# Kernel tuning notes

Hardware: AMD Instinct MI355X
Metric: run time of the kernel (lower is better)

The kernel has to match this reference:

```python
import jax, jax.numpy as jnp
import numpy as np

N = 50000
E = 800000
D_IN = 256
D_OUT = 256
EPS = 1.0 + 1e-06


def setup_inputs() -> dict:
    key = jax.random.key(0)
    ks = jax.random.split(key, 10)
    x = jax.random.normal(ks[0], (N, D_IN), dtype=jnp.float32)
    lower_indices = jax.random.randint(ks[1], (2, E), 0, N, dtype=jnp.int64)
    lower_values = jax.random.uniform(ks[2], (E,), dtype=jnp.float32)
    upper_indices = jax.random.randint(ks[3], (2, E), 0, N, dtype=jnp.int64)
    upper_values = jax.random.uniform(ks[4], (E,), dtype=jnp.float32)
    s = 1.0 / np.sqrt(D_IN)
    W_lower = jax.random.uniform(ks[5], (D_IN, D_OUT), jnp.float32, -s, s)
    att_lower = jax.random.uniform(ks[6], (2 * D_OUT,), jnp.float32, -s, s)
    W_upper = jax.random.uniform(ks[7], (D_IN, D_OUT), jnp.float32, -s, s)
    att_upper = jax.random.uniform(ks[8], (2 * D_OUT,), jnp.float32, -s, s)
    W_lin = jax.random.uniform(ks[9], (D_IN, D_OUT), jnp.float32, -s, s)
    return {"x": x, "lower_indices": lower_indices, "lower_values": lower_values,
            "upper_indices": upper_indices, "upper_values": upper_values,
            "W_lower": W_lower, "att_lower": att_lower,
            "W_upper": W_upper, "att_upper": att_upper, "W_lin": W_lin}


def can_conv(x, indices, values, W, att_weight):
    # x: [N, d_in]; indices: [2, E] (row=target i, col=source j); values: [E]
    n = x.shape[0]
    xm = x @ W                                    # [N, d_out]
    tgt, src = indices[0], indices[1]
    d = xm.shape[1]
    # attention: elu( [x_i ; x_j] . att_weight ) computed without concat
    score = jax.nn.elu(xm @ att_weight[:d])[tgt] + jax.nn.elu(0.0) * 0.0  # placeholder
    score = jax.nn.elu((xm @ att_weight[:d])[tgt] + (xm @ att_weight[d:])[src])  # [E]
    v = score * values                            # attention * neighborhood values
    # sparse row-wise softmax (per target index)
    m = jax.ops.segment_max(v, tgt, num_segments=n)
    e = jnp.exp(v - m[tgt])
    s = jax.ops.segment_sum(e, tgt, num_segments=n)
    a = e / s[tgt]                                # [E]
    # spmm: out[i] = sum_j a_ij * xm[j]
    return jax.ops.segment_sum(a[:, None] * xm[src], tgt, num_segments=n)


def reference(x, lower_indices, lower_values, upper_indices, upper_values,
              W_lower, att_lower, W_upper, att_upper, W_lin):
    lower_x = can_conv(x, lower_indices, lower_values, W_lower, att_lower)
    upper_x = can_conv(x, upper_indices, upper_values, W_upper, att_upper)
    w_x = (x @ W_lin) * EPS
    return jax.nn.relu(lower_x + upper_x + w_x)
```

## Files before the change

kernel.cpp:

```cpp
#include <hip/hip_runtime.h>
#include <hip/hip_bf16.h>


constexpr int N_NODES = 50000;
constexpr int N_EDGES = 800000;
constexpr int D = 256;
constexpr float EPSV = 1.0f + 1e-06f;

typedef __attribute__((ext_vector_type(8))) short short8;
typedef __attribute__((ext_vector_type(4))) float f32x4;

__device__ __forceinline__ unsigned short f2bf(float f) {
    unsigned int b = __float_as_uint(f);
    unsigned int r = (b + 0x7FFFu + ((b >> 16) & 1u)) >> 16;
    return (unsigned short)r;
}
__device__ __forceinline__ float bf2f(unsigned short u) {
    return __uint_as_float(((unsigned int)u) << 16);
}

__global__ __launch_bounds__(256) void prep_kernel(
    const float4* __restrict__ x, ushort4* __restrict__ xb, int n4,
    const float* __restrict__ W0, const float* __restrict__ W1,
    const float* __restrict__ W2, unsigned short* __restrict__ wbT,
    const int* __restrict__ il, const int* __restrict__ iu,
    int* __restrict__ cl, int* __restrict__ cu,
    int* __restrict__ rkl, int* __restrict__ rku)
{
    int gid = blockIdx.x * 256 + threadIdx.x;
    int gsz = gridDim.x * 256;
    for (int i = gid; i < n4; i += gsz) {
        float4 v = x[i];
        ushort4 o;
        o.x = f2bf(v.x); o.y = f2bf(v.y); o.z = f2bf(v.z); o.w = f2bf(v.w);
        xb[i] = o;
    }
    for (int i = gid; i < 3 * 65536; i += gsz) {
        int z = i >> 16, rem = i & 65535;
        int k = rem >> 8, n = rem & 255;
        const float* W = (z == 0) ? W0 : (z == 1) ? W1 : W2;
        wbT[(size_t)z * 65536 + (size_t)n * 256 + k] = f2bf(W[(size_t)k * 256 + n]);
    }
    for (int e = gid; e < N_EDGES; e += gsz) {
        rkl[e] = atomicAdd(&cl[il[e]], 1);
        rku[e] = atomicAdd(&cu[iu[e]], 1);
    }
}

__global__ __launch_bounds__(256) void gemm_lds_kernel(
    const unsigned short* __restrict__ xb, const unsigned short* __restrict__ wbT,
    unsigned short* __restrict__ xml, unsigned short* __restrict__ xmu,
    float* __restrict__ out, int M)
{
    const int wz = blockIdx.z;
    const int tid = threadIdx.x;
    const int w = tid >> 6, lane = tid & 63;
    const int r16 = lane & 15, g = lane >> 4;
    const int m0 = blockIdx.x * 128 + w * 32;
    const int n0 = blockIdx.y * 64;

    __shared__ short8 bs[8][4][64];
    {
        const unsigned short* wb = wbT + (size_t)wz * 65536;
        #pragma unroll
        for (int c = tid; c < 2048; c += 256) {
            int kt = c >> 8, nf = (c >> 6) & 3, l = c & 63;
            bs[kt][nf][l] = *reinterpret_cast<const short8*>(
                wb + (size_t)(n0 + nf * 16 + (l & 15)) * 256 + kt * 32 + 8 * (l >> 4));
        }
    }
    __syncthreads();

    const int ar0 = min(m0 + r16, M - 1);
    const int ar1 = min(m0 + 16 + r16, M - 1);
    const unsigned short* pa0 = xb + (size_t)ar0 * 256 + 8 * g;
    const unsigned short* pa1 = xb + (size_t)ar1 * 256 + 8 * g;

    f32x4 acc[2][4];
    #pragma unroll
    for (int mf = 0; mf < 2; ++mf)
        #pragma unroll
        for (int nf = 0; nf < 4; ++nf)
            acc[mf][nf] = (f32x4){0.f, 0.f, 0.f, 0.f};

    #pragma unroll
    for (int kt = 0; kt < 8; ++kt) {
        short8 a0 = *reinterpret_cast<const short8*>(pa0 + kt * 32);
        short8 a1 = *reinterpret_cast<const short8*>(pa1 + kt * 32);
        #pragma unroll
        for (int nf = 0; nf < 4; ++nf) {
            short8 bf = bs[kt][nf][lane];
            acc[0][nf] = __builtin_amdgcn_mfma_f32_16x16x32_bf16(a0, bf, acc[0][nf], 0, 0, 0);
            acc[1][nf] = __builtin_amdgcn_mfma_f32_16x16x32_bf16(a1, bf, acc[1][nf], 0, 0, 0);
        }
    }

    if (wz < 2) {
        unsigned short* dst = wz ? xmu : xml;
        #pragma unroll
        for (int mf = 0; mf < 2; ++mf)
            #pragma unroll
            for (int r = 0; r < 4; ++r) {
                int row = m0 + mf * 16 + g * 4 + r;
                if (row < M) {
                    #pragma unroll
                    for (int nf = 0; nf < 4; ++nf)
                        dst[(size_t)row * 256 + n0 + nf * 16 + r16] = f2bf(acc[mf][nf][r]);
                }
            }
    } else {
        #pragma unroll
        for (int mf = 0; mf < 2; ++mf)
            #pragma unroll
            for (int r = 0; r < 4; ++r) {
                int row = m0 + mf * 16 + g * 4 + r;
                if (row < M) {
                    #pragma unroll
                    for (int nf = 0; nf < 4; ++nf)
                        out[(size_t)row * 256 + n0 + nf * 16 + r16] = acc[mf][nf][r] * EPSV;
                }
            }
    }
}

__global__ __launch_bounds__(256) void att_both_kernel(
    const unsigned short* __restrict__ xml, const unsigned short* __restrict__ xmu,
    const float* __restrict__ att_l, const float* __restrict__ att_u,
    float* __restrict__ al, float* __restrict__ bl,
    float* __restrict__ au, float* __restrict__ bu, int n)
{
    int node = (int)((blockIdx.x * 256 + threadIdx.x) >> 6);
    int lane = threadIdx.x & 63;
    if (node >= n) return;
    int o = lane * 4;
    ushort4 ul = *reinterpret_cast<const ushort4*>(xml + (size_t)node * 256 + o);
    ushort4 uu = *reinterpret_cast<const ushort4*>(xmu + (size_t)node * 256 + o);
    float l0 = bf2f(ul.x), l1 = bf2f(ul.y), l2 = bf2f(ul.z), l3 = bf2f(ul.w);
    float u0 = bf2f(uu.x), u1 = bf2f(uu.y), u2 = bf2f(uu.z), u3 = bf2f(uu.w);
    float p[4];
    p[0] = l0 * att_l[o] + l1 * att_l[o + 1] + l2 * att_l[o + 2] + l3 * att_l[o + 3];
    p[1] = l0 * att_l[D + o] + l1 * att_l[D + o + 1] + l2 * att_l[D + o + 2] + l3 * att_l[D + o + 3];
    p[2] = u0 * att_u[o] + u1 * att_u[o + 1] + u2 * att_u[o + 2] + u3 * att_u[o + 3];
    p[3] = u0 * att_u[D + o] + u1 * att_u[D + o + 1] + u2 * att_u[D + o + 2] + u3 * att_u[D + o + 3];
    #pragma unroll
    for (int off = 32; off; off >>= 1)
        #pragma unroll
        for (int c = 0; c < 4; ++c)
            p[c] += __shfl_down(p[c], off);
    if (lane == 0) { al[node] = p[0]; bl[node] = p[1]; au[node] = p[2]; bu[node] = p[3]; }
}

__global__ __launch_bounds__(1024) void scan_local_kernel(
    const int* __restrict__ cnt0, int* __restrict__ ro0,
    const int* __restrict__ cnt1, int* __restrict__ ro1,
    int* __restrict__ bsum, int n)
{
    int c = blockIdx.y;
    const int* cnt = c ? cnt1 : cnt0;
    int* ro = c ? ro1 : ro0;
    __shared__ int sm[1024];
    int tid = threadIdx.x;
    int i = blockIdx.x * 1024 + tid;
    int v = (i < n) ? cnt[i] : 0;
    sm[tid] = v;
    __syncthreads();
    #pragma unroll
    for (int off = 1; off < 1024; off <<= 1) {
        int t = (tid >= off) ? sm[tid - off] : 0;
        __syncthreads();
        sm[tid] += t;
        __syncthreads();
    }
    if (i < n) ro[i] = sm[tid] - v;
    if (tid == 1023) bsum[c * 64 + blockIdx.x] = sm[1023];
}

__global__ __launch_bounds__(128) void scan_bsum_kernel(int* __restrict__ bsum, int nb)
{
    int c = threadIdx.x >> 6, lane = threadIdx.x & 63;
    int v = (lane < nb) ? bsum[c * 64 + lane] : 0;
    int orig = v;
    #pragma unroll
    for (int off = 1; off < 64; off <<= 1) {
        int t = __shfl_up(v, off);
        if (lane >= off) v += t;
    }
    if (lane < nb) bsum[c * 64 + lane] = v - orig;
}

__global__ __launch_bounds__(256) void scan_apply_kernel(
    int* __restrict__ ro0, int* __restrict__ ro1,
    const int* __restrict__ bsum, int n)
{
    int c = blockIdx.y;
    int* ro = c ? ro1 : ro0;
    int i = blockIdx.x * 256 + threadIdx.x;
    if (i < n) ro[i] += bsum[c * 64 + (i >> 10)];
    if (i == 0) ro[n] = N_EDGES;
}

__global__ __launch_bounds__(256) void scatter_kernel(
    const int* __restrict__ il, const float* __restrict__ vl,
    const int* __restrict__ rol, const int* __restrict__ rkl, int2* __restrict__ egl,
    const int* __restrict__ iu, const float* __restrict__ vu,
    const int* __restrict__ rou, const int* __restrict__ rku, int2* __restrict__ egu)
{
    int e = blockIdx.x * 256 + threadIdx.x;
    if (e >= N_EDGES) return;
    int2 p; p.x = il[N_EDGES + e]; p.y = __float_as_int(vl[e]);
    egl[rol[il[e]] + rkl[e]] = p;
    int2 q; q.x = iu[N_EDGES + e]; q.y = __float_as_int(vu[e]);
    egu[rou[iu[e]] + rku[e]] = q;
}

__device__ __forceinline__ float wave_sum(float v) {
    #pragma unroll
    for (int off = 32; off; off >>= 1) v += __shfl_xor(v, off);
    return v;
}

__device__ __forceinline__ void pv_accum(
    int lane, float invs, float evl, int srcl, int m,
    const unsigned short* __restrict__ xm, float4& acc)
{
    int t = 0;
    for (; t + 2 <= m; t += 2) {
        float w0 = __shfl(evl, t) * invs;
        int   s0 = __shfl(srcl, t);
        float w1 = __shfl(evl, t + 1) * invs;
        int   s1 = __shfl(srcl, t + 1);
        ushort4 u0 = *reinterpret_cast<const ushort4*>(xm + (size_t)s0 * 256 + lane * 4);
        ushort4 u1 = *reinterpret_cast<const ushort4*>(xm + (size_t)s1 * 256 + lane * 4);
        acc.x += w0 * bf2f(u0.x) + w1 * bf2f(u1.x);
        acc.y += w0 * bf2f(u0.y) + w1 * bf2f(u1.y);
        acc.z += w0 * bf2f(u0.z) + w1 * bf2f(u1.z);
        acc.w += w0 * bf2f(u0.w) + w1 * bf2f(u1.w);
    }
    if (t < m) {
        float w0 = __shfl(evl, t) * invs;
        int   s0 = __shfl(srcl, t);
        ushort4 u0 = *reinterpret_cast<const ushort4*>(xm + (size_t)s0 * 256 + lane * 4);
        acc.x += w0 * bf2f(u0.x);
        acc.y += w0 * bf2f(u0.y);
        acc.z += w0 * bf2f(u0.z);
        acc.w += w0 * bf2f(u0.w);
    }
}

__device__ __forceinline__ void conv_accum(
    int node, int lane,
    const int* __restrict__ ro, const int2* __restrict__ eg,
    const float* __restrict__ a, const float* __restrict__ b,
    const unsigned short* __restrict__ xm, float4& acc)
{
    int rs = ro[node], re = ro[node + 1];
    int deg = re - rs;
    if (deg <= 0) return;
    float ai = a[node];
    if (deg <= 64) {
        float evl = 0.f; int srcl = 0;
        if (lane < deg) {
            int2 p = eg[rs + lane];
            srcl = p.x;
            float xv = ai + b[srcl];
            float sc = (xv > 0.f) ? xv : (expf(xv) - 1.f);
            evl = expf(sc * __int_as_float(p.y));
        }
        float invs = 1.f / wave_sum(evl);
        pv_accum(lane, invs, evl, srcl, deg, xm, acc);
    } else {
        float s = 0.f;
        for (int c = rs; c < re; c += 64) {
            int m = min(64, re - c);
            float evl = 0.f;
            if (lane < m) {
                int2 p = eg[c + lane];
                float xv = ai + b[p.x];
                float sc = (xv > 0.f) ? xv : (expf(xv) - 1.f);
                evl = expf(sc * __int_as_float(p.y));
            }
            s += wave_sum(evl);
        }
        float invs = 1.f / s;
        for (int c = rs; c < re; c += 64) {
            int m = min(64, re - c);
            float evl = 0.f; int srcl = 0;
            if (lane < m) {
                int2 p = eg[c + lane];
                srcl = p.x;
                float xv = ai + b[srcl];
                float sc = (xv > 0.f) ? xv : (expf(xv) - 1.f);
                evl = expf(sc * __int_as_float(p.y));
            }
            pv_accum(lane, invs, evl, srcl, m, xm, acc);
        }
    }
}

__global__ __launch_bounds__(256) void gather_kernel(
    const int* __restrict__ rol, const int2* __restrict__ egl,
    const float* __restrict__ al, const float* __restrict__ bl,
    const unsigned short* __restrict__ xml,
    const int* __restrict__ rou, const int2* __restrict__ egu,
    const float* __restrict__ au, const float* __restrict__ bu,
    const unsigned short* __restrict__ xmu,
    float4* __restrict__ out)
{
    int node = (int)((blockIdx.x * 256 + threadIdx.x) >> 6);
    int lane = threadIdx.x & 63;
    if (node >= N_NODES) return;
    float4 acc = make_float4(0.f, 0.f, 0.f, 0.f);
    conv_accum(node, lane, rol, egl, al, bl, xml, acc);
    conv_accum(node, lane, rou, egu, au, bu, xmu, acc);
    float4 xw = out[(size_t)node * 64 + lane];
    acc.x = fmaxf(acc.x + xw.x, 0.f);
    acc.y = fmaxf(acc.y + xw.y, 0.f);
    acc.z = fmaxf(acc.z + xw.z, 0.f);
    acc.w = fmaxf(acc.w + xw.w, 0.f);
    out[(size_t)node * 64 + lane] = acc;
}

extern "C" void kernel_launch(void* const* d_in, const int* in_sizes, int n_in,
                              void* d_out, int out_size, void* d_ws, size_t ws_size,
                              hipStream_t stream)
{
    (void)in_sizes; (void)n_in; (void)out_size; (void)ws_size;
    const float* x        = (const float*)d_in[0];
    const int*   low_idx  = (const int*)  d_in[1];
    const float* low_vals = (const float*)d_in[2];
    const int*   up_idx   = (const int*)  d_in[3];
    const float* up_vals  = (const float*)d_in[4];
    const float* W_lower  = (const float*)d_in[5];
    const float* att_low  = (const float*)d_in[6];
    const float* W_upper  = (const float*)d_in[7];
    const float* att_up   = (const float*)d_in[8];
    const float* W_lin    = (const float*)d_in[9];
    float* out = (float*)d_out;

    char* ws = (char*)d_ws;
    size_t off = 0;
    auto alloc = [&](size_t bytes) {
        void* p = ws + off;
        off += (bytes + 255) & ~(size_t)255;
        return p;
    };
    unsigned short* xb     = (unsigned short*)alloc((size_t)N_NODES * D * 2);
    unsigned short* wbT    = (unsigned short*)alloc((size_t)3 * 256 * 256 * 2);
    unsigned short* xm_low = (unsigned short*)alloc((size_t)N_NODES * D * 2);
    unsigned short* xm_up  = (unsigned short*)alloc((size_t)N_NODES * D * 2);
    float* a_low  = (float*)alloc(N_NODES * 4);
    float* b_low  = (float*)alloc(N_NODES * 4);
    float* a_up   = (float*)alloc(N_NODES * 4);
    float* b_up   = (float*)alloc(N_NODES * 4);
    int* zero_blk = (int*)alloc(2 * N_NODES * 4);
    int* cnt_low = zero_blk;
    int* cnt_up  = zero_blk + N_NODES;
    int* rk_low  = (int*)alloc((size_t)N_EDGES * 4);
    int* rk_up   = (int*)alloc((size_t)N_EDGES * 4);
    int* ro_low  = (int*)alloc((N_NODES + 1) * 4);
    int* ro_up   = (int*)alloc((N_NODES + 1) * 4);
    int* bsum    = (int*)alloc(2 * 64 * 4);
    int2* eg_low = (int2*)alloc((size_t)N_EDGES * 8);
    int2* eg_up  = (int2*)alloc((size_t)N_EDGES * 8);

    hipMemsetAsync(zero_blk, 0, 2 * N_NODES * 4, stream);

    int n4 = N_NODES * D / 4;
    prep_kernel<<<2048, 256, 0, stream>>>(
        (const float4*)x, (ushort4*)xb, n4,
        W_lower, W_upper, W_lin, wbT,
        low_idx, up_idx, cnt_low, cnt_up, rk_low, rk_up);

    dim3 ggrid((N_NODES + 127) / 128, 4, 3);
    gemm_lds_kernel<<<ggrid, 256, 0, stream>>>(xb, wbT, xm_low, xm_up, out, N_NODES);

    int ablocks = (N_NODES + 3) / 4;
    att_both_kernel<<<ablocks, 256, 0, stream>>>(
        xm_low, xm_up, att_low, att_up, a_low, b_low, a_up, b_up, N_NODES);

    dim3 sgrid((N_NODES + 1023) / 1024, 2);
    scan_local_kernel<<<sgrid, 1024, 0, stream>>>(cnt_low, ro_low, cnt_up, ro_up,
                                                  bsum, N_NODES);
    scan_bsum_kernel<<<1, 128, 0, stream>>>(bsum, (N_NODES + 1023) / 1024);
    dim3 agrid((N_NODES + 255) / 256, 2);
    scan_apply_kernel<<<agrid, 256, 0, stream>>>(ro_low, ro_up, bsum, N_NODES);
    int eblocks = (N_EDGES + 255) / 256;
    scatter_kernel<<<eblocks, 256, 0, stream>>>(
        low_idx, low_vals, ro_low, rk_low, eg_low,
        up_idx,  up_vals,  ro_up,  rk_up,  eg_up);

    int gblocks = (N_NODES + 3) / 4;
    gather_kernel<<<gblocks, 256, 0, stream>>>(
        ro_low, eg_low, a_low, b_low, xm_low,
        ro_up,  eg_up,  a_up,  b_up,  xm_up,
        (float4*)out);
}
```

Before: 439.4 us.

## Fuse scan passes, merge attention with scatter, bf16 skip path, split gather waves

The three-kernel scan is replaced by a single decoupled-lookback scan that spins on per-block flags. The attention-score kernel and the edge scatter kernel are merged into one launch. The skip GEMM now writes a bf16 buffer instead of fp32 into the output, which cuts write and read traffic. The gather kernel gives the lower and upper convolutions separate waves and reduces them through LDS, and the gather inner loop is unrolled to four edges. The trade-offs are a spin-wait that assumes all scan blocks are co-resident, and bf16 rounding on the skip term.

```diff
diff --git a/kernel.cpp b/kernel.cpp
--- a/kernel.cpp
+++ b/kernel.cpp
@@ -50,7 +50,7 @@
 __global__ __launch_bounds__(256) void gemm_lds_kernel(
     const unsigned short* __restrict__ xb, const unsigned short* __restrict__ wbT,
     unsigned short* __restrict__ xml, unsigned short* __restrict__ xmu,
-    float* __restrict__ out, int M)
+    unsigned short* __restrict__ skipb, int M)
 {
     const int wz = blockIdx.z;
     const int tid = threadIdx.x;
@@ -95,72 +95,34 @@
         }
     }
 
-    if (wz < 2) {
-        unsigned short* dst = wz ? xmu : xml;
-        #pragma unroll
-        for (int mf = 0; mf < 2; ++mf)
-            #pragma unroll
-            for (int r = 0; r < 4; ++r) {
-                int row = m0 + mf * 16 + g * 4 + r;
-                if (row < M) {
-                    #pragma unroll
-                    for (int nf = 0; nf < 4; ++nf)
-                        dst[(size_t)row * 256 + n0 + nf * 16 + r16] = f2bf(acc[mf][nf][r]);
-                }
+    unsigned short* dst = (wz == 0) ? xml : (wz == 1) ? xmu : skipb;
+    const float scale = (wz == 2) ? EPSV : 1.0f;
+    #pragma unroll
+    for (int mf = 0; mf < 2; ++mf)
+        #pragma unroll
+        for (int r = 0; r < 4; ++r) {
+            int row = m0 + mf * 16 + g * 4 + r;
+            if (row < M) {
+                #pragma unroll
+                for (int nf = 0; nf < 4; ++nf)
+                    dst[(size_t)row * 256 + n0 + nf * 16 + r16] = f2bf(acc[mf][nf][r] * scale);
             }
-    } else {
-        #pragma unroll
-        for (int mf = 0; mf < 2; ++mf)
-            #pragma unroll
-            for (int r = 0; r < 4; ++r) {
-                int row = m0 + mf * 16 + g * 4 + r;
-                if (row < M) {
-                    #pragma unroll
-                    for (int nf = 0; nf < 4; ++nf)
-                        out[(size_t)row * 256 + n0 + nf * 16 + r16] = acc[mf][nf][r] * EPSV;
-                }
-            }
-    }
-}
-
-__global__ __launch_bounds__(256) void att_both_kernel(
-    const unsigned short* __restrict__ xml, const unsigned short* __restrict__ xmu,
-    const float* __restrict__ att_l, const float* __restrict__ att_u,
-    float* __restrict__ al, float* __restrict__ bl,
-    float* __restrict__ au, float* __restrict__ bu, int n)
-{
-    int node = (int)((blockIdx.x * 256 + threadIdx.x) >> 6);
-    int lane = threadIdx.x & 63;
-    if (node >= n) return;
-    int o = lane * 4;
-    ushort4 ul = *reinterpret_cast<const ushort4*>(xml + (size_t)node * 256 + o);
-    ushort4 uu = *reinterpret_cast<const ushort4*>(xmu + (size_t)node * 256 + o);
-    float l0 = bf2f(ul.x), l1 = bf2f(ul.y), l2 = bf2f(ul.z), l3 = bf2f(ul.w);
-    float u0 = bf2f(uu.x), u1 = bf2f(uu.y), u2 = bf2f(uu.z), u3 = bf2f(uu.w);
-    float p[4];
-    p[0] = l0 * att_l[o] + l1 * att_l[o + 1] + l2 * att_l[o + 2] + l3 * att_l[o + 3];
-    p[1] = l0 * att_l[D + o] + l1 * att_l[D + o + 1] + l2 * att_l[D + o + 2] + l3 * att_l[D + o + 3];
-    p[2] = u0 * att_u[o] + u1 * att_u[o + 1] + u2 * att_u[o + 2] + u3 * att_u[o + 3];
-    p[3] = u0 * att_u[D + o] + u1 * att_u[D + o + 1] + u2 * att_u[D + o + 2] + u3 * att_u[D + o + 3];
-    #pragma unroll
-    for (int off = 32; off; off >>= 1)
-        #pragma unroll
-        for (int c = 0; c < 4; ++c)
-            p[c] += __shfl_down(p[c], off);
-    if (lane == 0) { al[node] = p[0]; bl[node] = p[1]; au[node] = p[2]; bu[node] = p[3]; }
-}
-
-__global__ __launch_bounds__(1024) void scan_local_kernel(
+        }
+}
+
+__global__ __launch_bounds__(1024) void scan_kernel(
     const int* __restrict__ cnt0, int* __restrict__ ro0,
     const int* __restrict__ cnt1, int* __restrict__ ro1,
-    int* __restrict__ bsum, int n)
+    int* __restrict__ fv, int n)
 {
     int c = blockIdx.y;
     const int* cnt = c ? cnt1 : cnt0;
     int* ro = c ? ro1 : ro0;
+    int b = blockIdx.x;
     __shared__ int sm[1024];
+    __shared__ int s_prefix;
     int tid = threadIdx.x;
-    int i = blockIdx.x * 1024 + tid;
+    int i = b * 1024 + tid;
     int v = (i < n) ? cnt[i] : 0;
     sm[tid] = v;
     __syncthreads();
@@ -171,46 +133,64 @@
         sm[tid] += t;
         __syncthreads();
     }
-    if (i < n) ro[i] = sm[tid] - v;
-    if (tid == 1023) bsum[c * 64 + blockIdx.x] = sm[1023];
-}
-
-__global__ __launch_bounds__(128) void scan_bsum_kernel(int* __restrict__ bsum, int nb)
-{
-    int c = threadIdx.x >> 6, lane = threadIdx.x & 63;
-    int v = (lane < nb) ? bsum[c * 64 + lane] : 0;
-    int orig = v;
-    #pragma unroll
-    for (int off = 1; off < 64; off <<= 1) {
-        int t = __shfl_up(v, off);
-        if (lane >= off) v += t;
-    }
-    if (lane < nb) bsum[c * 64 + lane] = v - orig;
-}
-
-__global__ __launch_bounds__(256) void scan_apply_kernel(
-    int* __restrict__ ro0, int* __restrict__ ro1,
-    const int* __restrict__ bsum, int n)
-{
-    int c = blockIdx.y;
-    int* ro = c ? ro1 : ro0;
-    int i = blockIdx.x * 256 + threadIdx.x;
-    if (i < n) ro[i] += bsum[c * 64 + (i >> 10)];
-    if (i == 0) ro[n] = N_EDGES;
-}
-
-__global__ __launch_bounds__(256) void scatter_kernel(
+    int total = sm[1023];
+    if (tid == 0) atomicExch(&fv[c * 64 + b], total + 1);
+    if (tid < 64) {
+        int p = 0;
+        if (tid < b) {
+            int f;
+            while ((f = atomicAdd(&fv[c * 64 + tid], 0)) == 0) {}
+            p = f - 1;
+        }
+        #pragma unroll
+        for (int off = 32; off; off >>= 1) p += __shfl_xor(p, off);
+        if (tid == 0) s_prefix = p;
+    }
+    __syncthreads();
+    int prefix = s_prefix;
+    if (i < n) ro[i] = prefix + sm[tid] - v;
+    if (tid == 0 && b == (int)gridDim.x - 1) ro[n] = prefix + total;
+}
+
+__global__ __launch_bounds__(256) void att_scatter_kernel(
+    const unsigned short* __restrict__ xml, const unsigned short* __restrict__ xmu,
+    const float* __restrict__ att_l, const float* __restrict__ att_u,
+    float* __restrict__ al, float* __restrict__ bl,
+    float* __restrict__ au, float* __restrict__ bu, int n_ab,
     const int* __restrict__ il, const float* __restrict__ vl,
     const int* __restrict__ rol, const int* __restrict__ rkl, int2* __restrict__ egl,
     const int* __restrict__ iu, const float* __restrict__ vu,
     const int* __restrict__ rou, const int* __restrict__ rku, int2* __restrict__ egu)
 {
-    int e = blockIdx.x * 256 + threadIdx.x;
-    if (e >= N_EDGES) return;
-    int2 p; p.x = il[N_EDGES + e]; p.y = __float_as_int(vl[e]);
-    egl[rol[il[e]] + rkl[e]] = p;
-    int2 q; q.x = iu[N_EDGES + e]; q.y = __float_as_int(vu[e]);
-    egu[rou[iu[e]] + rku[e]] = q;
+    int bx = (int)blockIdx.x;
+    if (bx < n_ab) {
+        int node = (int)((bx * 256 + threadIdx.x) >> 6);
+        int lane = threadIdx.x & 63;
+        if (node >= N_NODES) return;
+        int o = lane * 4;
+        ushort4 ul = *reinterpret_cast<const ushort4*>(xml + (size_t)node * 256 + o);
+        ushort4 uu = *reinterpret_cast<const ushort4*>(xmu + (size_t)node * 256 + o);
+        float l0 = bf2f(ul.x), l1 = bf2f(ul.y), l2 = bf2f(ul.z), l3 = bf2f(ul.w);
+        float u0 = bf2f(uu.x), u1 = bf2f(uu.y), u2 = bf2f(uu.z), u3 = bf2f(uu.w);
+        float p[4];
+        p[0] = l0 * att_l[o] + l1 * att_l[o + 1] + l2 * att_l[o + 2] + l3 * att_l[o + 3];
+        p[1] = l0 * att_l[D + o] + l1 * att_l[D + o + 1] + l2 * att_l[D + o + 2] + l3 * att_l[D + o + 3];
+        p[2] = u0 * att_u[o] + u1 * att_u[o + 1] + u2 * att_u[o + 2] + u3 * att_u[o + 3];
+        p[3] = u0 * att_u[D + o] + u1 * att_u[D + o + 1] + u2 * att_u[D + o + 2] + u3 * att_u[D + o + 3];
+        #pragma unroll
+        for (int off = 32; off; off >>= 1)
+            #pragma unroll
+            for (int c = 0; c < 4; ++c)
+                p[c] += __shfl_down(p[c], off);
+        if (lane == 0) { al[node] = p[0]; bl[node] = p[1]; au[node] = p[2]; bu[node] = p[3]; }
+    } else {
+        int e = (bx - n_ab) * 256 + threadIdx.x;
+        if (e >= N_EDGES) return;
+        int2 p; p.x = il[N_EDGES + e]; p.y = __float_as_int(vl[e]);
+        egl[rol[il[e]] + rkl[e]] = p;
+        int2 q; q.x = iu[N_EDGES + e]; q.y = __float_as_int(vu[e]);
+        egu[rou[iu[e]] + rku[e]] = q;
+    }
 }
 
 __device__ __forceinline__ float wave_sum(float v) {
@@ -224,19 +204,25 @@
     const unsigned short* __restrict__ xm, float4& acc)
 {
     int t = 0;
-    for (; t + 2 <= m; t += 2) {
-        float w0 = __shfl(evl, t) * invs;
-        int   s0 = __shfl(srcl, t);
+    for (; t + 4 <= m; t += 4) {
+        float w0 = __shfl(evl, t)     * invs;
         float w1 = __shfl(evl, t + 1) * invs;
-        int   s1 = __shfl(srcl, t + 1);
+        float w2 = __shfl(evl, t + 2) * invs;
+        float w3 = __shfl(evl, t + 3) * invs;
+        int s0 = __shfl(srcl, t);
+        int s1 = __shfl(srcl, t + 1);
+        int s2 = __shfl(srcl, t + 2);
+        int s3 = __shfl(srcl, t + 3);
         ushort4 u0 = *reinterpret_cast<const ushort4*>(xm + (size_t)s0 * 256 + lane * 4);
         ushort4 u1 = *reinterpret_cast<const ushort4*>(xm + (size_t)s1 * 256 + lane * 4);
-        acc.x += w0 * bf2f(u0.x) + w1 * bf2f(u1.x);
-        acc.y += w0 * bf2f(u0.y) + w1 * bf2f(u1.y);
-        acc.z += w0 * bf2f(u0.z) + w1 * bf2f(u1.z);
-        acc.w += w0 * bf2f(u0.w) + w1 * bf2f(u1.w);
-    }
-    if (t < m) {
+        ushort4 u2 = *reinterpret_cast<const ushort4*>(xm + (size_t)s2 * 256 + lane * 4);
+        ushort4 u3 = *reinterpret_cast<const ushort4*>(xm + (size_t)s3 * 256 + lane * 4);
+        acc.x += w0 * bf2f(u0.x) + w1 * bf2f(u1.x) + w2 * bf2f(u2.x) + w3 * bf2f(u3.x);
+        acc.y += w0 * bf2f(u0.y) + w1 * bf2f(u1.y) + w2 * bf2f(u2.y) + w3 * bf2f(u3.y);
+        acc.z += w0 * bf2f(u0.z) + w1 * bf2f(u1.z) + w2 * bf2f(u2.z) + w3 * bf2f(u3.z);
+        acc.w += w0 * bf2f(u0.w) + w1 * bf2f(u1.w) + w2 * bf2f(u2.w) + w3 * bf2f(u3.w);
+    }
+    for (; t < m; ++t) {
         float w0 = __shfl(evl, t) * invs;
         int   s0 = __shfl(srcl, t);
         ushort4 u0 = *reinterpret_cast<const ushort4*>(xm + (size_t)s0 * 256 + lane * 4);
@@ -304,20 +290,30 @@
     const int* __restrict__ rou, const int2* __restrict__ egu,
     const float* __restrict__ au, const float* __restrict__ bu,
     const unsigned short* __restrict__ xmu,
-    float4* __restrict__ out)
-{
-    int node = (int)((blockIdx.x * 256 + threadIdx.x) >> 6);
-    int lane = threadIdx.x & 63;
-    if (node >= N_NODES) return;
+    const unsigned short* __restrict__ skipb, float4* __restrict__ out)
+{
+    int tid = threadIdx.x;
+    int slot = tid >> 7;
+    int conv = (tid >> 6) & 1;
+    int lane = tid & 63;
+    int node = blockIdx.x * 2 + slot;
+    __shared__ float4 red[2][64];
     float4 acc = make_float4(0.f, 0.f, 0.f, 0.f);
-    conv_accum(node, lane, rol, egl, al, bl, xml, acc);
-    conv_accum(node, lane, rou, egu, au, bu, xmu, acc);
-    float4 xw = out[(size_t)node * 64 + lane];
-    acc.x = fmaxf(acc.x + xw.x, 0.f);
-    acc.y = fmaxf(acc.y + xw.y, 0.f);
-    acc.z = fmaxf(acc.z + xw.z, 0.f);
-    acc.w = fmaxf(acc.w + xw.w, 0.f);
-    out[(size_t)node * 64 + lane] = acc;
+    if (node < N_NODES) {
+        if (conv == 0) conv_accum(node, lane, rol, egl, al, bl, xml, acc);
+        else           conv_accum(node, lane, rou, egu, au, bu, xmu, acc);
+    }
+    if (conv == 1) red[slot][lane] = acc;
+    __syncthreads();
+    if (conv == 0 && node < N_NODES) {
+        float4 o = red[slot][lane];
+        ushort4 sk = *reinterpret_cast<const ushort4*>(skipb + (size_t)node * 256 + lane * 4);
+        acc.x = fmaxf(acc.x + o.x + bf2f(sk.x), 0.f);
+        acc.y = fmaxf(acc.y + o.y + bf2f(sk.y), 0.f);
+        acc.z = fmaxf(acc.z + o.z + bf2f(sk.z), 0.f);
+        acc.w = fmaxf(acc.w + o.w + bf2f(sk.w), 0.f);
+        out[(size_t)node * 64 + lane] = acc;
+    }
 }
 
 extern "C" void kernel_launch(void* const* d_in, const int* in_sizes, int n_in,
@@ -348,22 +344,23 @@
     unsigned short* wbT    = (unsigned short*)alloc((size_t)3 * 256 * 256 * 2);
     unsigned short* xm_low = (unsigned short*)alloc((size_t)N_NODES * D * 2);
     unsigned short* xm_up  = (unsigned short*)alloc((size_t)N_NODES * D * 2);
+    unsigned short* skipb  = (unsigned short*)alloc((size_t)N_NODES * D * 2);
     float* a_low  = (float*)alloc(N_NODES * 4);
     float* b_low  = (float*)alloc(N_NODES * 4);
     float* a_up   = (float*)alloc(N_NODES * 4);
     float* b_up   = (float*)alloc(N_NODES * 4);
-    int* zero_blk = (int*)alloc(2 * N_NODES * 4);
+    int* zero_blk = (int*)alloc((2 * N_NODES + 128) * 4);
     int* cnt_low = zero_blk;
     int* cnt_up  = zero_blk + N_NODES;
+    int* fv      = zero_blk + 2 * N_NODES;
     int* rk_low  = (int*)alloc((size_t)N_EDGES * 4);
     int* rk_up   = (int*)alloc((size_t)N_EDGES * 4);
     int* ro_low  = (int*)alloc((N_NODES + 1) * 4);
     int* ro_up   = (int*)alloc((N_NODES + 1) * 4);
-    int* bsum    = (int*)alloc(2 * 64 * 4);
     int2* eg_low = (int2*)alloc((size_t)N_EDGES * 8);
     int2* eg_up  = (int2*)alloc((size_t)N_EDGES * 8);
 
-    hipMemsetAsync(zero_blk, 0, 2 * N_NODES * 4, stream);
+    hipMemsetAsync(zero_blk, 0, (2 * N_NODES + 128) * 4, stream);
 
     int n4 = N_NODES * D / 4;
     prep_kernel<<<2048, 256, 0, stream>>>(
@@ -372,26 +369,21 @@
         low_idx, up_idx, cnt_low, cnt_up, rk_low, rk_up);
 
     dim3 ggrid((N_NODES + 127) / 128, 4, 3);
-    gemm_lds_kernel<<<ggrid, 256, 0, stream>>>(xb, wbT, xm_low, xm_up, out, N_NODES);
+    gemm_lds_kernel<<<ggrid, 256, 0, stream>>>(xb, wbT, xm_low, xm_up, skipb, N_NODES);
+
+    dim3 sgrid((N_NODES + 1023) / 1024, 2);
+    scan_kernel<<<sgrid, 1024, 0, stream>>>(cnt_low, ro_low, cnt_up, ro_up, fv, N_NODES);
 
     int ablocks = (N_NODES + 3) / 4;
-    att_both_kernel<<<ablocks, 256, 0, stream>>>(
-        xm_low, xm_up, att_low, att_up, a_low, b_low, a_up, b_up, N_NODES);
-
-    dim3 sgrid((N_NODES + 1023) / 1024, 2);
-    scan_local_kernel<<<sgrid, 1024, 0, stream>>>(cnt_low, ro_low, cnt_up, ro_up,
-                                                  bsum, N_NODES);
-    scan_bsum_kernel<<<1, 128, 0, stream>>>(bsum, (N_NODES + 1023) / 1024);
-    dim3 agrid((N_NODES + 255) / 256, 2);
-    scan_apply_kernel<<<agrid, 256, 0, stream>>>(ro_low, ro_up, bsum, N_NODES);
     int eblocks = (N_EDGES + 255) / 256;
-    scatter_kernel<<<eblocks, 256, 0, stream>>>(
+    att_scatter_kernel<<<ablocks + eblocks, 256, 0, stream>>>(
+        xm_low, xm_up, att_low, att_up, a_low, b_low, a_up, b_up, ablocks,
         low_idx, low_vals, ro_low, rk_low, eg_low,
         up_idx,  up_vals,  ro_up,  rk_up,  eg_up);
 
-    int gblocks = (N_NODES + 3) / 4;
+    int gblocks = (N_NODES + 1) / 2;
     gather_kernel<<<gblocks, 256, 0, stream>>>(
         ro_low, eg_low, a_low, b_low, xm_low,
         ro_up,  eg_up,  a_up,  b_up,  xm_up,
-        (float4*)out);
-}
+        skipb, (float4*)out);
+}
```

After: 454.7 us. 3.5% more time.

## Fuse three GEMMs per block, precompute edge exps in scatter, split gather per conv

Applied to the files above, without the earlier changes.

The GEMM now loads each A tile into registers once and loops over the three weight matrices, so the x tile is not re-read per matrix. The skip projection is written as bf16 to a scratch buffer instead of fp32 into the output. The scatter kernel computes the ELU/exp edge weights up front, so the gather no longer does per-edge attention math and random reads of b. The gather assigns one wave per conv per node, sums the two results through LDS, and unrolls the SpMM by four. Storing the skip term in bf16 adds rounding error and removes one fp32 read-modify-write of the output. The exp is taken without subtracting the segment max, which could overflow for large scores.

```diff
diff --git a/kernel.cpp b/kernel.cpp
--- a/kernel.cpp
+++ b/kernel.cpp
@@ -47,12 +47,11 @@
     }
 }
 
-__global__ __launch_bounds__(256) void gemm_lds_kernel(
+__global__ __launch_bounds__(256) void gemm_zreg_kernel(
     const unsigned short* __restrict__ xb, const unsigned short* __restrict__ wbT,
     unsigned short* __restrict__ xml, unsigned short* __restrict__ xmu,
-    float* __restrict__ out, int M)
-{
-    const int wz = blockIdx.z;
+    unsigned short* __restrict__ skipb, int M)
+{
     const int tid = threadIdx.x;
     const int w = tid >> 6, lane = tid & 63;
     const int r16 = lane & 15, g = lane >> 4;
@@ -60,43 +59,50 @@
     const int n0 = blockIdx.y * 64;
 
     __shared__ short8 bs[8][4][64];
-    {
-        const unsigned short* wb = wbT + (size_t)wz * 65536;
-        #pragma unroll
-        for (int c = tid; c < 2048; c += 256) {
-            int kt = c >> 8, nf = (c >> 6) & 3, l = c & 63;
-            bs[kt][nf][l] = *reinterpret_cast<const short8*>(
-                wb + (size_t)(n0 + nf * 16 + (l & 15)) * 256 + kt * 32 + 8 * (l >> 4));
-        }
-    }
-    __syncthreads();
 
     const int ar0 = min(m0 + r16, M - 1);
     const int ar1 = min(m0 + 16 + r16, M - 1);
     const unsigned short* pa0 = xb + (size_t)ar0 * 256 + 8 * g;
     const unsigned short* pa1 = xb + (size_t)ar1 * 256 + 8 * g;
-
-    f32x4 acc[2][4];
-    #pragma unroll
-    for (int mf = 0; mf < 2; ++mf)
-        #pragma unroll
-        for (int nf = 0; nf < 4; ++nf)
-            acc[mf][nf] = (f32x4){0.f, 0.f, 0.f, 0.f};
-
+    short8 af[2][8];
     #pragma unroll
     for (int kt = 0; kt < 8; ++kt) {
-        short8 a0 = *reinterpret_cast<const short8*>(pa0 + kt * 32);
-        short8 a1 = *reinterpret_cast<const short8*>(pa1 + kt * 32);
+        af[0][kt] = *reinterpret_cast<const short8*>(pa0 + kt * 32);
+        af[1][kt] = *reinterpret_cast<const short8*>(pa1 + kt * 32);
+    }
+
+    for (int z = 0; z < 3; ++z) {
+        __syncthreads();
+        {
+            const unsigned short* wb = wbT + (size_t)z * 65536;
+            #pragma unroll
+            for (int c = tid; c < 2048; c += 256) {
+                int kt = c >> 8, nf = (c >> 6) & 3, l = c & 63;
+                bs[kt][nf][l] = *reinterpret_cast<const short8*>(
+                    wb + (size_t)(n0 + nf * 16 + (l & 15)) * 256 + kt * 32 + 8 * (l >> 4));
+            }
+        }
+        __syncthreads();
+
+        f32x4 acc[2][4];
         #pragma unroll
-        for (int nf = 0; nf < 4; ++nf) {
-            short8 bf = bs[kt][nf][lane];
-            acc[0][nf] = __builtin_amdgcn_mfma_f32_16x16x32_bf16(a0, bf, acc[0][nf], 0, 0, 0);
-            acc[1][nf] = __builtin_amdgcn_mfma_f32_16x16x32_bf16(a1, bf, acc[1][nf], 0, 0, 0);
+        for (int mf = 0; mf < 2; ++mf)
+            #pragma unroll
+            for (int nf = 0; nf < 4; ++nf)
+                acc[mf][nf] = (f32x4){0.f, 0.f, 0.f, 0.f};
+
+        #pragma unroll
+        for (int kt = 0; kt < 8; ++kt) {
+            #pragma unroll
+            for (int nf = 0; nf < 4; ++nf) {
+                short8 bf = bs[kt][nf][lane];
+                acc[0][nf] = __builtin_amdgcn_mfma_f32_16x16x32_bf16(af[0][kt], bf, acc[0][nf], 0, 0, 0);
+                acc[1][nf] = __builtin_amdgcn_mfma_f32_16x16x32_bf16(af[1][kt], bf, acc[1][nf], 0, 0, 0);
+            }
         }
-    }
-
-    if (wz < 2) {
-        unsigned short* dst = wz ? xmu : xml;
+
+        unsigned short* dst = (z == 0) ? xml : (z == 1) ? xmu : skipb;
+        const float scale = (z == 2) ? EPSV : 1.0f;
         #pragma unroll
         for (int mf = 0; mf < 2; ++mf)
             #pragma unroll
@@ -105,19 +111,7 @@
                 if (row < M) {
                     #pragma unroll
                     for (int nf = 0; nf < 4; ++nf)
-                        dst[(size_t)row * 256 + n0 + nf * 16 + r16] = f2bf(acc[mf][nf][r]);
-                }
-            }
-    } else {
-        #pragma unroll
-        for (int mf = 0; mf < 2; ++mf)
-            #pragma unroll
-            for (int r = 0; r < 4; ++r) {
-                int row = m0 + mf * 16 + g * 4 + r;
-                if (row < M) {
-                    #pragma unroll
-                    for (int nf = 0; nf < 4; ++nf)
-                        out[(size_t)row * 256 + n0 + nf * 16 + r16] = acc[mf][nf][r] * EPSV;
+                        dst[(size_t)row * 256 + n0 + nf * 16 + r16] = f2bf(acc[mf][nf][r] * scale);
                 }
             }
     }
@@ -199,18 +193,34 @@
     if (i == 0) ro[n] = N_EDGES;
 }
 
-__global__ __launch_bounds__(256) void scatter_kernel(
+__global__ __launch_bounds__(256) void scatter_ev_kernel(
     const int* __restrict__ il, const float* __restrict__ vl,
-    const int* __restrict__ rol, const int* __restrict__ rkl, int2* __restrict__ egl,
+    const int* __restrict__ rol, const int* __restrict__ rkl,
+    const float* __restrict__ al, const float* __restrict__ blv,
+    int2* __restrict__ egl,
     const int* __restrict__ iu, const float* __restrict__ vu,
-    const int* __restrict__ rou, const int* __restrict__ rku, int2* __restrict__ egu)
+    const int* __restrict__ rou, const int* __restrict__ rku,
+    const float* __restrict__ au, const float* __restrict__ buv,
+    int2* __restrict__ egu)
 {
     int e = blockIdx.x * 256 + threadIdx.x;
     if (e >= N_EDGES) return;
-    int2 p; p.x = il[N_EDGES + e]; p.y = __float_as_int(vl[e]);
-    egl[rol[il[e]] + rkl[e]] = p;
-    int2 q; q.x = iu[N_EDGES + e]; q.y = __float_as_int(vu[e]);
-    egu[rou[iu[e]] + rku[e]] = q;
+    {
+        int t = il[e], s = il[N_EDGES + e];
+        float xv = al[t] + blv[s];
+        float sc = (xv > 0.f) ? xv : (expf(xv) - 1.f);
+        float ev = expf(sc * vl[e]);
+        int2 p; p.x = s; p.y = __float_as_int(ev);
+        egl[rol[t] + rkl[e]] = p;
+    }
+    {
+        int t = iu[e], s = iu[N_EDGES + e];
+        float xv = au[t] + buv[s];
+        float sc = (xv > 0.f) ? xv : (expf(xv) - 1.f);
+        float ev = expf(sc * vu[e]);
+        int2 q; q.x = s; q.y = __float_as_int(ev);
+        egu[rou[t] + rku[e]] = q;
+    }
 }
 
 __device__ __forceinline__ float wave_sum(float v) {
@@ -224,19 +234,25 @@
     const unsigned short* __restrict__ xm, float4& acc)
 {
     int t = 0;
-    for (; t + 2 <= m; t += 2) {
-        float w0 = __shfl(evl, t) * invs;
-        int   s0 = __shfl(srcl, t);
+    for (; t + 4 <= m; t += 4) {
+        float w0 = __shfl(evl, t)     * invs;
         float w1 = __shfl(evl, t + 1) * invs;
-        int   s1 = __shfl(srcl, t + 1);
+        float w2 = __shfl(evl, t + 2) * invs;
+        float w3 = __shfl(evl, t + 3) * invs;
+        int s0 = __shfl(srcl, t);
+        int s1 = __shfl(srcl, t + 1);
+        int s2 = __shfl(srcl, t + 2);
+        int s3 = __shfl(srcl, t + 3);
         ushort4 u0 = *reinterpret_cast<const ushort4*>(xm + (size_t)s0 * 256 + lane * 4);
         ushort4 u1 = *reinterpret_cast<const ushort4*>(xm + (size_t)s1 * 256 + lane * 4);
-        acc.x += w0 * bf2f(u0.x) + w1 * bf2f(u1.x);
-        acc.y += w0 * bf2f(u0.y) + w1 * bf2f(u1.y);
-        acc.z += w0 * bf2f(u0.z) + w1 * bf2f(u1.z);
-        acc.w += w0 * bf2f(u0.w) + w1 * bf2f(u1.w);
-    }
-    if (t < m) {
+        ushort4 u2 = *reinterpret_cast<const ushort4*>(xm + (size_t)s2 * 256 + lane * 4);
+        ushort4 u3 = *reinterpret_cast<const ushort4*>(xm + (size_t)s3 * 256 + lane * 4);
+        acc.x += w0 * bf2f(u0.x) + w1 * bf2f(u1.x) + w2 * bf2f(u2.x) + w3 * bf2f(u3.x);
+        acc.y += w0 * bf2f(u0.y) + w1 * bf2f(u1.y) + w2 * bf2f(u2.y) + w3 * bf2f(u3.y);
+        acc.z += w0 * bf2f(u0.z) + w1 * bf2f(u1.z) + w2 * bf2f(u2.z) + w3 * bf2f(u3.z);
+        acc.w += w0 * bf2f(u0.w) + w1 * bf2f(u1.w) + w2 * bf2f(u2.w) + w3 * bf2f(u3.w);
+    }
+    for (; t < m; ++t) {
         float w0 = __shfl(evl, t) * invs;
         int   s0 = __shfl(srcl, t);
         ushort4 u0 = *reinterpret_cast<const ushort4*>(xm + (size_t)s0 * 256 + lane * 4);
@@ -250,21 +266,17 @@
 __device__ __forceinline__ void conv_accum(
     int node, int lane,
     const int* __restrict__ ro, const int2* __restrict__ eg,
-    const float* __restrict__ a, const float* __restrict__ b,
     const unsigned short* __restrict__ xm, float4& acc)
 {
     int rs = ro[node], re = ro[node + 1];
     int deg = re - rs;
     if (deg <= 0) return;
-    float ai = a[node];
     if (deg <= 64) {
         float evl = 0.f; int srcl = 0;
         if (lane < deg) {
             int2 p = eg[rs + lane];
             srcl = p.x;
-            float xv = ai + b[srcl];
-            float sc = (xv > 0.f) ? xv : (expf(xv) - 1.f);
-            evl = expf(sc * __int_as_float(p.y));
+            evl = __int_as_float(p.y);
         }
         float invs = 1.f / wave_sum(evl);
         pv_accum(lane, invs, evl, srcl, deg, xm, acc);
@@ -272,13 +284,7 @@
         float s = 0.f;
         for (int c = rs; c < re; c += 64) {
             int m = min(64, re - c);
-            float evl = 0.f;
-            if (lane < m) {
-                int2 p = eg[c + lane];
-                float xv = ai + b[p.x];
-                float sc = (xv > 0.f) ? xv : (expf(xv) - 1.f);
-                evl = expf(sc * __int_as_float(p.y));
-            }
+            float evl = (lane < m) ? __int_as_float(eg[c + lane].y) : 0.f;
             s += wave_sum(evl);
         }
         float invs = 1.f / s;
@@ -288,9 +294,7 @@
             if (lane < m) {
                 int2 p = eg[c + lane];
                 srcl = p.x;
-                float xv = ai + b[srcl];
-                float sc = (xv > 0.f) ? xv : (expf(xv) - 1.f);
-                evl = expf(sc * __int_as_float(p.y));
+                evl = __int_as_float(p.y);
             }
             pv_accum(lane, invs, evl, srcl, m, xm, acc);
         }
@@ -299,25 +303,33 @@
 
 __global__ __launch_bounds__(256) void gather_kernel(
     const int* __restrict__ rol, const int2* __restrict__ egl,
-    const float* __restrict__ al, const float* __restrict__ bl,
     const unsigned short* __restrict__ xml,
     const int* __restrict__ rou, const int2* __restrict__ egu,
-    const float* __restrict__ au, const float* __restrict__ bu,
     const unsigned short* __restrict__ xmu,
-    float4* __restrict__ out)
-{
-    int node = (int)((blockIdx.x * 256 + threadIdx.x) >> 6);
-    int lane = threadIdx.x & 63;
-    if (node >= N_NODES) return;
+    const unsigned short* __restrict__ skipb, float4* __restrict__ out)
+{
+    int tid = threadIdx.x;
+    int slot = tid >> 7;
+    int conv = (tid >> 6) & 1;
+    int lane = tid & 63;
+    int node = blockIdx.x * 2 + slot;
+    __shared__ float4 red[2][64];
     float4 acc = make_float4(0.f, 0.f, 0.f, 0.f);
-    conv_accum(node, lane, rol, egl, al, bl, xml, acc);
-    conv_accum(node, lane, rou, egu, au, bu, xmu, acc);
-    float4 xw = out[(size_t)node * 64 + lane];
-    acc.x = fmaxf(acc.x + xw.x, 0.f);
-    acc.y = fmaxf(acc.y + xw.y, 0.f);
-    acc.z = fmaxf(acc.z + xw.z, 0.f);
-    acc.w = fmaxf(acc.w + xw.w, 0.f);
-    out[(size_t)node * 64 + lane] = acc;
+    if (node < N_NODES) {
+        if (conv == 0) conv_accum(node, lane, rol, egl, xml, acc);
+        else           conv_accum(node, lane, rou, egu, xmu, acc);
+    }
+    if (conv == 1) red[slot][lane] = acc;
+    __syncthreads();
+    if (conv == 0 && node < N_NODES) {
+        float4 o = red[slot][lane];
+        ushort4 sk = *reinterpret_cast<const ushort4*>(skipb + (size_t)node * 256 + lane * 4);
+        acc.x = fmaxf(acc.x + o.x + bf2f(sk.x), 0.f);
+        acc.y = fmaxf(acc.y + o.y + bf2f(sk.y), 0.f);
+        acc.z = fmaxf(acc.z + o.z + bf2f(sk.z), 0.f);
+        acc.w = fmaxf(acc.w + o.w + bf2f(sk.w), 0.f);
+        out[(size_t)node * 64 + lane] = acc;
+    }
 }
 
 extern "C" void kernel_launch(void* const* d_in, const int* in_sizes, int n_in,
@@ -348,6 +360,7 @@
     unsigned short* wbT    = (unsigned short*)alloc((size_t)3 * 256 * 256 * 2);
     unsigned short* xm_low = (unsigned short*)alloc((size_t)N_NODES * D * 2);
     unsigned short* xm_up  = (unsigned short*)alloc((size_t)N_NODES * D * 2);
+    unsigned short* skipb  = (unsigned short*)alloc((size_t)N_NODES * D * 2);
     float* a_low  = (float*)alloc(N_NODES * 4);
     float* b_low  = (float*)alloc(N_NODES * 4);
     float* a_up   = (float*)alloc(N_NODES * 4);
@@ -371,8 +384,8 @@
         W_lower, W_upper, W_lin, wbT,
         low_idx, up_idx, cnt_low, cnt_up, rk_low, rk_up);
 
-    dim3 ggrid((N_NODES + 127) / 128, 4, 3);
-    gemm_lds_kernel<<<ggrid, 256, 0, stream>>>(xb, wbT, xm_low, xm_up, out, N_NODES);
+    dim3 ggrid((N_NODES + 127) / 128, 4);
+    gemm_zreg_kernel<<<ggrid, 256, 0, stream>>>(xb, wbT, xm_low, xm_up, skipb, N_NODES);
 
     int ablocks = (N_NODES + 3) / 4;
     att_both_kernel<<<ablocks, 256, 0, stream>>>(
@@ -384,14 +397,15 @@
     scan_bsum_kernel<<<1, 128, 0, stream>>>(bsum, (N_NODES + 1023) / 1024);
     dim3 agrid((N_NODES + 255) / 256, 2);
     scan_apply_kernel<<<agrid, 256, 0, stream>>>(ro_low, ro_up, bsum, N_NODES);
+
     int eblocks = (N_EDGES + 255) / 256;
-    scatter_kernel<<<eblocks, 256, 0, stream>>>(
-        low_idx, low_vals, ro_low, rk_low, eg_low,
-        up_idx,  up_vals,  ro_up,  rk_up,  eg_up);
-
-    int gblocks = (N_NODES + 3) / 4;
+    scatter_ev_kernel<<<eblocks, 256, 0, stream>>>(
+        low_idx, low_vals, ro_low, rk_low, a_low, b_low, eg_low,
+        up_idx,  up_vals,  ro_up,  rk_up,  a_up,  b_up,  eg_up);
+
+    int gblocks = (N_NODES + 1) / 2;
     gather_kernel<<<gblocks, 256, 0, stream>>>(
-        ro_low, eg_low, a_low, b_low, xm_low,
-        ro_up,  eg_up,  a_up,  b_up,  xm_up,
-        (float4*)out);
-}
+        ro_low, eg_low, xm_low,
+        ro_up,  eg_up,  xm_up,
+        skipb, (float4*)out);
+}
```

After: 450.1 us. 2.4% more time.
